# Optimization experiments

Hardware: AMD Instinct MI355X
Metric: run time of the kernel (lower is better)

Reference implementation:

```python
import jax, jax.numpy as jnp
import numpy as np

IN_FEATURES = 512
OUT_FEATURES = 512
GRID_SIZE = 8
SPLINE_ORDER = 3


def make_grid():
    # grid has grid_size + 2*spline_order + 1 knots in [-1, 1]
    return jnp.linspace(-1.0, 1.0, GRID_SIZE + 2 * SPLINE_ORDER + 1, dtype=jnp.float32)


def b_splines(x, grid):
    # x: (N, in)  ->  bases: (N, in, grid_size + spline_order)
    x = jnp.clip(x, -2.0, 2.0)[..., None]  # (N, in, 1)
    bases = ((x >= grid[:-1]) & (x < grid[1:])).astype(x.dtype)
    for k in range(1, SPLINE_ORDER + 1):
        denom1 = grid[k:-1] - grid[:-(k + 1)]
        denom1 = jnp.where(jnp.abs(denom1) < 1e-8, jnp.ones_like(denom1), denom1)
        denom2 = grid[k + 1:] - grid[1:-k]
        denom2 = jnp.where(jnp.abs(denom2) < 1e-8, jnp.ones_like(denom2), denom2)
        bases = ((x - grid[:-(k + 1)]) / denom1 * bases[..., :-1]
                 + (grid[k + 1:] - x) / denom2 * bases[..., 1:])
    return bases


def setup_inputs() -> dict:
    key = jax.random.key(0)
    kx, kb, ks = jax.random.split(key, 3)
    x = jax.random.normal(kx, (8192, IN_FEATURES), dtype=jnp.float32)
    # xavier_uniform with gain=0.5 for base_weight
    limit = 0.5 * np.sqrt(6.0 / (IN_FEATURES + OUT_FEATURES))
    base_weight = jax.random.uniform(kb, (OUT_FEATURES, IN_FEATURES), dtype=jnp.float32,
                                     minval=-limit, maxval=limit)
    spline_weight = 0.01 * jax.random.normal(
        ks, (OUT_FEATURES, IN_FEATURES, GRID_SIZE + SPLINE_ORDER), dtype=jnp.float32)
    return {"x": x, "base_weight": base_weight, "spline_weight": spline_weight}


def reference(x, base_weight, spline_weight):
    grid = make_grid()
    base_out = x @ base_weight.T                      # (N, out)
    basis = b_splines(x, grid)                        # (N, in, G+K)
    spline_out = jnp.einsum('bij,oij->bo', basis, spline_weight)
    return base_out + spline_out
```

## Files before the change

### kernel.cpp

```cpp
#include <hip/hip_runtime.h>
#include <stdint.h>

#define IN_F 512
#define OUT_F 512
#define NROWS 8192
#define NSLOT 12
#define KTOT (IN_F * NSLOT)
#define K16S (KTOT / 16)
#define BK 96
#define NITER (KTOT / BK)
#define KSPLIT 4
#define APAD_ROW 120
#define SW_ROW (IN_F * 11)

typedef __bf16 bf16x8 __attribute__((ext_vector_type(8)));
typedef float f32x16 __attribute__((ext_vector_type(16)));

__device__ ushort g_Wb[K16S * 16 * 64 * 8];

__device__ __forceinline__ ushort f2bf(float f) {
    uint32_t u = __builtin_bit_cast(uint32_t, f);
    u += 0x7FFFu + ((u >> 16) & 1u);
    return (ushort)(u >> 16);
}

__global__ __launch_bounds__(64) void prep_weights(const float* __restrict__ bw,
                                                   const float* __restrict__ sw) {
    __shared__ __align__(16) ushort kcol[KTOT];
    const int o    = blockIdx.x;
    const int lane = threadIdx.x;
    const float* swr = sw + (size_t)o * SW_ROW;

    #pragma unroll
    for (int i = 0; i < 22; ++i) {
        int idx4 = lane + i * 64;
        float4 v = ((const float4*)swr)[idx4];
        uint p = (uint)idx4 * 4;
        #pragma unroll
        for (int c = 0; c < 4; ++c) {
            uint pc = p + c;
            uint f = pc / 11u;
            uint j = pc - f * 11u;
            float val = (c == 0) ? v.x : (c == 1) ? v.y : (c == 2) ? v.z : v.w;
            kcol[f * NSLOT + j] = f2bf(val);
        }
    }
    #pragma unroll
    for (int i = 0; i < 8; ++i) {
        int f = lane + i * 64;
        kcol[f * NSLOT + 11] = f2bf(bw[(size_t)o * IN_F + f]);
    }
    __syncthreads();

    const int nt = o >> 5;
    const int ol = o & 31;
    #pragma unroll
    for (int c = 0; c < 12; ++c) {
        int chunk = lane + c * 64;
        int k16   = chunk >> 1;
        int half  = chunk & 1;
        uint4 val = *(const uint4*)&kcol[k16 * 16 + half * 8];
        ((uint4*)g_Wb)[((size_t)(k16 * 16 + nt)) * 64 + ol + 32 * half] = val;
    }
}

__global__ __launch_bounds__(256, 3) void kan_gemm(const float* __restrict__ x,
                                                   float* __restrict__ out) {
    __shared__ __align__(16) ushort As[128 * APAD_ROW];

    const int t    = threadIdx.x;
    const int lane = t & 63;
    const int w    = t >> 6;
    const int ln31 = lane & 31;
    const int half = lane >> 5;

    const int bx = blockIdx.x;
    const int ng = bx & 3;
    const int kp = (bx >> 2) & 3;
    const int mb = bx >> 4;
    const int row_base = mb * 128;
    const int col_base = ng * 128;
    const int wm = (w & 1) * 64;
    const int wn = (w >> 1) * 64;

    const int sm = t >> 1;
    const int fh = t & 1;

    f32x16 acc[2][2] = {};

    const int it0 = kp * (NITER / KSPLIT);
    #pragma unroll 1
    for (int ii = 0; ii < NITER / KSPLIT; ++ii) {
        const int it = it0 + ii;
        uint4 breg[6][2];
        #pragma unroll
        for (int ks = 0; ks < 6; ++ks) {
            int k16g = it * 6 + ks;
            #pragma unroll
            for (int nt = 0; nt < 2; ++nt) {
                int ntg = ng * 4 + (w >> 1) * 2 + nt;
                breg[ks][nt] = ((const uint4*)g_Wb)[((size_t)k16g * 16 + ntg) * 64 + lane];
            }
        }
        const float4 xv = *(const float4*)&x[(size_t)(row_base + sm) * IN_F + it * 8 + fh * 4];

        __syncthreads();

        {
            #pragma unroll
            for (int c = 0; c < 4; ++c) {
                float xx = (c == 0) ? xv.x : (c == 1) ? xv.y : (c == 2) ? xv.z : xv.w;
                float wpos = (xx + 1.0f) * 7.0f;
                float fi = floorf(wpos);
                int   i  = (int)fi;
                float u  = wpos - fi;
                bool inr = (xx >= -1.0f) && (xx < 1.0f);
                int   q  = i - 3;
                float um = 1.0f - u;
                float uu = u * u, u3 = uu * u;
                const float C6 = 1.0f / 6.0f;
                float s0 = (inr && q >= 0) ? C6 : 0.0f;
                float s1 = (inr && q >= -1 && q <= 9) ? C6 : 0.0f;
                float s2 = (inr && q >= -2 && q <= 8) ? C6 : 0.0f;
                float s3 = (inr && q <= 7) ? C6 : 0.0f;
                uint b0 = f2bf(um * um * um * s0);
                uint b1 = f2bf((3.0f * u3 - 6.0f * uu + 4.0f) * s1);
                uint b2 = f2bf((-3.0f * u3 + 3.0f * uu + 3.0f * u + 1.0f) * s2);
                uint b3 = f2bf(u3 * s3);
                int r  = q & 1;
                int e0 = q & ~1;
                uint P0 = r ? (b0 << 16)        : (b0 | (b1 << 16));
                uint P1 = r ? (b1 | (b2 << 16)) : (b2 | (b3 << 16));
                uint P2 = r ? b3                : 0u;
                uint p[6];
                #pragma unroll
                for (int pi = 0; pi < 6; ++pi) {
                    int d = 2 * pi - e0;
                    p[pi] = (d == 0) ? P0 : (d == 2) ? P1 : (d == 4) ? P2 : 0u;
                }
                p[5] = (p[5] & 0xFFFFu) | ((uint)f2bf(xx) << 16);
                ushort* rowp = &As[sm * APAD_ROW + (fh * 4 + c) * NSLOT];
                uint2 w0; w0.x = p[0]; w0.y = p[1];
                uint2 w1; w1.x = p[2]; w1.y = p[3];
                uint2 w2; w2.x = p[4]; w2.y = p[5];
                *(uint2*)&rowp[0] = w0;
                *(uint2*)&rowp[4] = w1;
                *(uint2*)&rowp[8] = w2;
            }
        }

        __syncthreads();

        #pragma unroll
        for (int ks = 0; ks < 6; ++ks) {
            uint4 a0 = *(const uint4*)&As[(wm + ln31) * APAD_ROW + ks * 16 + half * 8];
            uint4 a1 = *(const uint4*)&As[(wm + 32 + ln31) * APAD_ROW + ks * 16 + half * 8];
            bf16x8 af0 = __builtin_bit_cast(bf16x8, a0);
            bf16x8 af1 = __builtin_bit_cast(bf16x8, a1);
            bf16x8 bf0 = __builtin_bit_cast(bf16x8, breg[ks][0]);
            bf16x8 bf1 = __builtin_bit_cast(bf16x8, breg[ks][1]);
            acc[0][0] = __builtin_amdgcn_mfma_f32_32x32x16_bf16(af0, bf0, acc[0][0], 0, 0, 0);
            acc[0][1] = __builtin_amdgcn_mfma_f32_32x32x16_bf16(af0, bf1, acc[0][1], 0, 0, 0);
            acc[1][0] = __builtin_amdgcn_mfma_f32_32x32x16_bf16(af1, bf0, acc[1][0], 0, 0, 0);
            acc[1][1] = __builtin_amdgcn_mfma_f32_32x32x16_bf16(af1, bf1, acc[1][1], 0, 0, 0);
        }
    }

    #pragma unroll
    for (int mt = 0; mt < 2; ++mt) {
        #pragma unroll
        for (int nt = 0; nt < 2; ++nt) {
            int rb = row_base + wm + mt * 32 + 4 * half;
            int cc = col_base + wn + nt * 32 + ln31;
            #pragma unroll
            for (int reg = 0; reg < 16; ++reg) {
                int rr = rb + (reg & 3) + 8 * (reg >> 2);
                unsafeAtomicAdd(&out[(size_t)rr * OUT_F + cc], acc[mt][nt][reg]);
            }
        }
    }
}

extern "C" void kernel_launch(void* const* d_in, const int* in_sizes, int n_in,
                              void* d_out, int out_size, void* d_ws, size_t ws_size,
                              hipStream_t stream) {
    const float* x  = (const float*)d_in[0];
    const float* bw = (const float*)d_in[1];
    const float* sw = (const float*)d_in[2];
    float* out = (float*)d_out;
    hipMemsetAsync(out, 0, (size_t)out_size * sizeof(float), stream);
    hipLaunchKernelGGL(prep_weights, dim3(512), dim3(64), 0, stream, bw, sw);
    hipLaunchKernelGGL(kan_gemm, dim3(64 * 4 * KSPLIT), dim3(256), 0, stream, x, out);
}
```

Baseline: 184.0 us.

## Widen GEMM tile to full output width and restructure weight prep blocks

The GEMM block now covers all 512 output columns with 8 waves of 512 threads, each wave computing 128x64. Each block builds the spline basis tile for its 128 rows once, where before the basis was recomputed for each of four column groups. The weight prep kernel moves to 128 blocks of 256 threads, each handling 32 outputs by 64 features, so global writes are more coalesced. The trade-offs are fewer blocks (256), more accumulator registers per wave, and four A-fragment LDS reads per k-step.

```diff
diff --git a/kernel.cpp b/kernel.cpp
--- a/kernel.cpp
+++ b/kernel.cpp
@@ -7,11 +7,11 @@
 #define NSLOT 12
 #define KTOT (IN_F * NSLOT)
 #define K16S (KTOT / 16)
-#define BK 96
-#define NITER (KTOT / BK)
 #define KSPLIT 4
+#define ITERS 16
 #define APAD_ROW 120
 #define SW_ROW (IN_F * 11)
+#define KC_PAD 776
 
 typedef __bf16 bf16x8 __attribute__((ext_vector_type(8)));
 typedef float f32x16 __attribute__((ext_vector_type(16)));
@@ -24,47 +24,57 @@
     return (ushort)(u >> 16);
 }
 
-__global__ __launch_bounds__(64) void prep_weights(const float* __restrict__ bw,
-                                                   const float* __restrict__ sw) {
-    __shared__ __align__(16) ushort kcol[KTOT];
-    const int o    = blockIdx.x;
-    const int lane = threadIdx.x;
-    const float* swr = sw + (size_t)o * SW_ROW;
-
-    #pragma unroll
-    for (int i = 0; i < 22; ++i) {
-        int idx4 = lane + i * 64;
-        float4 v = ((const float4*)swr)[idx4];
-        uint p = (uint)idx4 * 4;
-        #pragma unroll
-        for (int c = 0; c < 4; ++c) {
-            uint pc = p + c;
-            uint f = pc / 11u;
-            uint j = pc - f * 11u;
-            float val = (c == 0) ? v.x : (c == 1) ? v.y : (c == 2) ? v.z : v.w;
-            kcol[f * NSLOT + j] = f2bf(val);
-        }
-    }
-    #pragma unroll
-    for (int i = 0; i < 8; ++i) {
-        int f = lane + i * 64;
-        kcol[f * NSLOT + 11] = f2bf(bw[(size_t)o * IN_F + f]);
+__global__ __launch_bounds__(256) void prep_weights(const float* __restrict__ bw,
+                                                    const float* __restrict__ sw) {
+    __shared__ __align__(16) ushort kcol[32 * KC_PAD];
+    const int t  = threadIdx.x;
+    const int nt = blockIdx.x & 15;
+    const int kg = blockIdx.x >> 4;
+    const int o0 = nt * 32;
+    const int f0 = kg * 64;
+
+    {
+        const int o_l = t >> 3;
+        const int tr  = t & 7;
+        const float* swr = sw + (size_t)(o0 + o_l) * SW_ROW + (size_t)f0 * 11;
+        #pragma unroll
+        for (int i = 0; i < 22; ++i) {
+            int p4 = tr + i * 8;
+            float4 v = ((const float4*)swr)[p4];
+            uint pos = (uint)p4 * 4;
+            #pragma unroll
+            for (int c = 0; c < 4; ++c) {
+                uint pc = pos + c;
+                uint fl = pc / 11u;
+                uint j  = pc - fl * 11u;
+                float val = (c == 0) ? v.x : (c == 1) ? v.y : (c == 2) ? v.z : v.w;
+                kcol[o_l * KC_PAD + fl * NSLOT + j] = f2bf(val);
+            }
+        }
+        #pragma unroll
+        for (int i = 0; i < 8; ++i) {
+            int fl = tr + i * 8;
+            kcol[o_l * KC_PAD + fl * NSLOT + 11] =
+                f2bf(bw[(size_t)(o0 + o_l) * IN_F + f0 + fl]);
+        }
     }
     __syncthreads();
 
-    const int nt = o >> 5;
-    const int ol = o & 31;
-    #pragma unroll
-    for (int c = 0; c < 12; ++c) {
-        int chunk = lane + c * 64;
-        int k16   = chunk >> 1;
-        int half  = chunk & 1;
-        uint4 val = *(const uint4*)&kcol[k16 * 16 + half * 8];
-        ((uint4*)g_Wb)[((size_t)(k16 * 16 + nt)) * 64 + ol + 32 * half] = val;
-    }
-}
-
-__global__ __launch_bounds__(256, 3) void kan_gemm(const float* __restrict__ x,
+    {
+        const int ol = t & 31;
+        const int ph = t >> 5;
+        #pragma unroll
+        for (int i = 0; i < 12; ++i) {
+            int idx  = ph + i * 8;
+            int k16l = idx >> 1;
+            int half = idx & 1;
+            uint4 val = *(const uint4*)&kcol[ol * KC_PAD + k16l * 16 + half * 8];
+            ((uint4*)g_Wb)[((size_t)((kg * 48 + k16l) * 16 + nt)) * 64 + half * 32 + ol] = val;
+        }
+    }
+}
+
+__global__ __launch_bounds__(512, 2) void kan_gemm(const float* __restrict__ x,
                                                    float* __restrict__ out) {
     __shared__ __align__(16) ushort As[128 * APAD_ROW];
 
@@ -75,103 +85,100 @@
     const int half = lane >> 5;
 
     const int bx = blockIdx.x;
-    const int ng = bx & 3;
-    const int kp = (bx >> 2) & 3;
-    const int mb = bx >> 4;
+    const int mb = bx & 63;
+    const int kp = bx >> 6;
     const int row_base = mb * 128;
-    const int col_base = ng * 128;
-    const int wm = (w & 1) * 64;
-    const int wn = (w >> 1) * 64;
-
-    const int sm = t >> 1;
-    const int fh = t & 1;
-
-    f32x16 acc[2][2] = {};
-
-    const int it0 = kp * (NITER / KSPLIT);
+    const int wn = w * 64;
+
+    const int sm = t >> 2;
+    const int fh = t & 3;
+
+    f32x16 acc[4][2] = {};
+
     #pragma unroll 1
-    for (int ii = 0; ii < NITER / KSPLIT; ++ii) {
-        const int it = it0 + ii;
+    for (int ii = 0; ii < ITERS; ++ii) {
+        const int fbase = kp * 128 + ii * 8;
         uint4 breg[6][2];
         #pragma unroll
         for (int ks = 0; ks < 6; ++ks) {
-            int k16g = it * 6 + ks;
+            int k16g = kp * 96 + ii * 6 + ks;
             #pragma unroll
             for (int nt = 0; nt < 2; ++nt) {
-                int ntg = ng * 4 + (w >> 1) * 2 + nt;
+                int ntg = w * 2 + nt;
                 breg[ks][nt] = ((const uint4*)g_Wb)[((size_t)k16g * 16 + ntg) * 64 + lane];
             }
         }
-        const float4 xv = *(const float4*)&x[(size_t)(row_base + sm) * IN_F + it * 8 + fh * 4];
+        const float2 xv = *(const float2*)&x[(size_t)(row_base + sm) * IN_F + fbase + fh * 2];
 
         __syncthreads();
 
-        {
-            #pragma unroll
-            for (int c = 0; c < 4; ++c) {
-                float xx = (c == 0) ? xv.x : (c == 1) ? xv.y : (c == 2) ? xv.z : xv.w;
-                float wpos = (xx + 1.0f) * 7.0f;
-                float fi = floorf(wpos);
-                int   i  = (int)fi;
-                float u  = wpos - fi;
-                bool inr = (xx >= -1.0f) && (xx < 1.0f);
-                int   q  = i - 3;
-                float um = 1.0f - u;
-                float uu = u * u, u3 = uu * u;
-                const float C6 = 1.0f / 6.0f;
-                float s0 = (inr && q >= 0) ? C6 : 0.0f;
-                float s1 = (inr && q >= -1 && q <= 9) ? C6 : 0.0f;
-                float s2 = (inr && q >= -2 && q <= 8) ? C6 : 0.0f;
-                float s3 = (inr && q <= 7) ? C6 : 0.0f;
-                uint b0 = f2bf(um * um * um * s0);
-                uint b1 = f2bf((3.0f * u3 - 6.0f * uu + 4.0f) * s1);
-                uint b2 = f2bf((-3.0f * u3 + 3.0f * uu + 3.0f * u + 1.0f) * s2);
-                uint b3 = f2bf(u3 * s3);
-                int r  = q & 1;
-                int e0 = q & ~1;
-                uint P0 = r ? (b0 << 16)        : (b0 | (b1 << 16));
-                uint P1 = r ? (b1 | (b2 << 16)) : (b2 | (b3 << 16));
-                uint P2 = r ? b3                : 0u;
-                uint p[6];
+        #pragma unroll
+        for (int c = 0; c < 2; ++c) {
+            float xx = c ? xv.y : xv.x;
+            float wpos = (xx + 1.0f) * 7.0f;
+            float fi = floorf(wpos);
+            int   i  = (int)fi;
+            float u  = wpos - fi;
+            bool inr = (xx >= -1.0f) && (xx < 1.0f);
+            int   q  = i - 3;
+            float um = 1.0f - u;
+            float uu = u * u, u3 = uu * u;
+            const float C6 = 1.0f / 6.0f;
+            float s0 = (inr && q >= 0) ? C6 : 0.0f;
+            float s1 = (inr && q >= -1 && q <= 9) ? C6 : 0.0f;
+            float s2 = (inr && q >= -2 && q <= 8) ? C6 : 0.0f;
+            float s3 = (inr && q <= 7) ? C6 : 0.0f;
+            uint b0 = f2bf(um * um * um * s0);
+            uint b1 = f2bf((3.0f * u3 - 6.0f * uu + 4.0f) * s1);
+            uint b2 = f2bf((-3.0f * u3 + 3.0f * uu + 3.0f * u + 1.0f) * s2);
+            uint b3 = f2bf(u3 * s3);
+            int r  = q & 1;
+            int e0 = q & ~1;
+            uint P0 = r ? (b0 << 16)        : (b0 | (b1 << 16));
+            uint P1 = r ? (b1 | (b2 << 16)) : (b2 | (b3 << 16));
+            uint P2 = r ? b3                : 0u;
+            uint p[6];
+            #pragma unroll
+            for (int pi = 0; pi < 6; ++pi) {
+                int d = 2 * pi - e0;
+                p[pi] = (d == 0) ? P0 : (d == 2) ? P1 : (d == 4) ? P2 : 0u;
+            }
+            p[5] = (p[5] & 0xFFFFu) | ((uint)f2bf(xx) << 16);
+            ushort* rowp = &As[sm * APAD_ROW + (fh * 2 + c) * NSLOT];
+            uint2 w0; w0.x = p[0]; w0.y = p[1];
+            uint2 w1; w1.x = p[2]; w1.y = p[3];
+            uint2 w2; w2.x = p[4]; w2.y = p[5];
+            *(uint2*)&rowp[0] = w0;
+            *(uint2*)&rowp[4] = w1;
+            *(uint2*)&rowp[8] = w2;
+        }
+
+        __syncthreads();
+
+        #pragma unroll
+        for (int ks = 0; ks < 6; ++ks) {
+            uint4 a[4];
+            #pragma unroll
+            for (int mt = 0; mt < 4; ++mt)
+                a[mt] = *(const uint4*)&As[(mt * 32 + ln31) * APAD_ROW + ks * 16 + half * 8];
+            #pragma unroll
+            for (int mt = 0; mt < 4; ++mt) {
+                bf16x8 af = __builtin_bit_cast(bf16x8, a[mt]);
                 #pragma unroll
-                for (int pi = 0; pi < 6; ++pi) {
-                    int d = 2 * pi - e0;
-                    p[pi] = (d == 0) ? P0 : (d == 2) ? P1 : (d == 4) ? P2 : 0u;
+                for (int nt = 0; nt < 2; ++nt) {
+                    bf16x8 bf = __builtin_bit_cast(bf16x8, breg[ks][nt]);
+                    acc[mt][nt] = __builtin_amdgcn_mfma_f32_32x32x16_bf16(af, bf, acc[mt][nt], 0, 0, 0);
                 }
-                p[5] = (p[5] & 0xFFFFu) | ((uint)f2bf(xx) << 16);
-                ushort* rowp = &As[sm * APAD_ROW + (fh * 4 + c) * NSLOT];
-                uint2 w0; w0.x = p[0]; w0.y = p[1];
-                uint2 w1; w1.x = p[2]; w1.y = p[3];
-                uint2 w2; w2.x = p[4]; w2.y = p[5];
-                *(uint2*)&rowp[0] = w0;
-                *(uint2*)&rowp[4] = w1;
-                *(uint2*)&rowp[8] = w2;
-            }
-        }
-
-        __syncthreads();
-
-        #pragma unroll
-        for (int ks = 0; ks < 6; ++ks) {
-            uint4 a0 = *(const uint4*)&As[(wm + ln31) * APAD_ROW + ks * 16 + half * 8];
-            uint4 a1 = *(const uint4*)&As[(wm + 32 + ln31) * APAD_ROW + ks * 16 + half * 8];
-            bf16x8 af0 = __builtin_bit_cast(bf16x8, a0);
-            bf16x8 af1 = __builtin_bit_cast(bf16x8, a1);
-            bf16x8 bf0 = __builtin_bit_cast(bf16x8, breg[ks][0]);
-            bf16x8 bf1 = __builtin_bit_cast(bf16x8, breg[ks][1]);
-            acc[0][0] = __builtin_amdgcn_mfma_f32_32x32x16_bf16(af0, bf0, acc[0][0], 0, 0, 0);
-            acc[0][1] = __builtin_amdgcn_mfma_f32_32x32x16_bf16(af0, bf1, acc[0][1], 0, 0, 0);
-            acc[1][0] = __builtin_amdgcn_mfma_f32_32x32x16_bf16(af1, bf0, acc[1][0], 0, 0, 0);
-            acc[1][1] = __builtin_amdgcn_mfma_f32_32x32x16_bf16(af1, bf1, acc[1][1], 0, 0, 0);
+            }
         }
     }
 
     #pragma unroll
-    for (int mt = 0; mt < 2; ++mt) {
+    for (int mt = 0; mt < 4; ++mt) {
         #pragma unroll
         for (int nt = 0; nt < 2; ++nt) {
-            int rb = row_base + wm + mt * 32 + 4 * half;
-            int cc = col_base + wn + nt * 32 + ln31;
+            int rb = row_base + mt * 32 + 4 * half;
+            int cc = wn + nt * 32 + ln31;
             #pragma unroll
             for (int reg = 0; reg < 16; ++reg) {
                 int rr = rb + (reg & 3) + 8 * (reg >> 2);
@@ -189,6 +196,6 @@
     const float* sw = (const float*)d_in[2];
     float* out = (float*)d_out;
     hipMemsetAsync(out, 0, (size_t)out_size * sizeof(float), stream);
-    hipLaunchKernelGGL(prep_weights, dim3(512), dim3(64), 0, stream, bw, sw);
-    hipLaunchKernelGGL(kan_gemm, dim3(64 * 4 * KSPLIT), dim3(256), 0, stream, x, out);
-}
+    hipLaunchKernelGGL(prep_weights, dim3(128), dim3(256), 0, stream, bw, sw);
+    hipLaunchKernelGGL(kan_gemm, dim3(64 * KSPLIT), dim3(512), 0, stream, x, out);
+}
```

Measured after the change: 174.2 us. -5.3%, faster.
